# Kernel tuning notes

Measured on AMD Instinct MI355X. Metric: run time of the kernel, lower is better.

The kernel has to match this reference:

```python
import jax, jax.numpy as jnp
import numpy as np

QLEN, MLEN, D, H = 1024, 1024, 1024, 16
DH = D // H
KLEN = QLEN + MLEN
SCALE = 1.0 / np.sqrt(DH).astype(np.float32)
W_STD = 0.02


def setup_inputs() -> dict:
    key = jax.random.key(0)
    ks = jax.random.split(key, 14)
    inputs = jax.random.normal(ks[0], (QLEN, 1, D), jnp.float32)
    r = jax.random.normal(ks[1], (KLEN, D), jnp.float32)
    u = jax.random.normal(ks[2], (H, DH), jnp.float32) * W_STD
    v = jax.random.normal(ks[3], (H, DH), jnp.float32) * W_STD
    mem = jax.random.normal(ks[4], (MLEN, 1, D), jnp.float32)
    # causal mask over concatenated [mem, inputs] keys: True = masked
    attn_mask = jnp.triu(jnp.ones((QLEN, KLEN), bool), k=MLEN + 1)
    W_qkv = jax.random.normal(ks[5], (3 * D, D), jnp.float32) * W_STD
    W_r = jax.random.normal(ks[6], (D, D), jnp.float32) * W_STD
    W_o = jax.random.normal(ks[7], (D, D), jnp.float32) * W_STD
    W_ih = jax.random.normal(ks[8], (3 * D, D), jnp.float32) * W_STD
    W_hh = jax.random.normal(ks[9], (3 * D, D), jnp.float32) * W_STD
    b_ih = jnp.zeros((3 * D,), jnp.float32)
    b_hh = jnp.zeros((3 * D,), jnp.float32)
    h0 = jnp.zeros((1, 1, D), jnp.float32)  # GRU hidden, forces batch=1
    return {"inputs": inputs, "r": r, "u": u, "v": v, "attn_mask": attn_mask,
            "mem": mem, "W_qkv": W_qkv, "W_r": W_r, "W_o": W_o,
            "W_ih": W_ih, "W_hh": W_hh, "b_ih": b_ih, "b_hh": b_hh, "h0": h0}


def _rel_shift(x):
    # Transformer-XL relative shift; x: [qlen, klen, b, n]
    q, k, b, n = x.shape
    zp = jnp.zeros((q, 1, b, n), x.dtype)
    xp = jnp.concatenate([zp, x], axis=1)          # [q, k+1, b, n]
    xp = xp.reshape(k + 1, q, b, n)[1:]            # drop first row
    return xp.reshape(q, k, b, n)


def reference(inputs, r, u, v, attn_mask, mem, W_qkv, W_r, W_o,
              W_ih, W_hh, b_ih, b_hh, h0):
    qlen, b, d = inputs.shape
    cat = jnp.concatenate([mem, inputs], axis=0)        # [klen, b, d]
    klen = cat.shape[0]
    w_heads = cat @ W_qkv.T                             # [klen, b, 3d]
    q_h, k_h, v_h = jnp.split(w_heads, 3, axis=-1)
    q_h = q_h[-qlen:].reshape(qlen, b, H, DH)
    k_h = k_h.reshape(klen, b, H, DH)
    v_h = v_h.reshape(klen, b, H, DH)
    r_k = (r @ W_r.T).reshape(klen, H, DH)              # relative key heads

    AC = jnp.einsum('ibnd,jbnd->ijbn', q_h + u, k_h)    # content score
    BD = _rel_shift(jnp.einsum('ibnd,jnd->ijbn', q_h + v, r_k))  # position score
    score = (AC + BD) * SCALE                           # [q, k, b, n]
    score = jnp.where(attn_mask[:, :, None, None], jnp.float32(-1e30), score)
    probs = jax.nn.softmax(score, axis=1)

    attn_vec = jnp.einsum('ijbn,jbnd->ibnd', probs, v_h).reshape(qlen, b, d)
    y = attn_vec @ W_o.T                                # [q, b, d]

    # 1-layer GRU over time (PyTorch gate order r, z, n)
    x_proj = y @ W_ih.T + b_ih                          # [q, b, 3d]

    def step(h, xt):
        gh = h @ W_hh.T + b_hh
        xr, xz, xn = jnp.split(xt, 3, axis=-1)
        hr, hz, hn = jnp.split(gh, 3, axis=-1)
        rg = jax.nn.sigmoid(xr + hr)
        zg = jax.nn.sigmoid(xz + hz)
        ng = jnp.tanh(xn + rg * hn)
        h_new = (1.0 - zg) * ng + zg * h
        return h_new, h_new

    _, ys = jax.lax.scan(step, h0[0], x_proj)           # h0[0]: [b, d]
    return ys, probs
```

## Files before the change

kernel.cpp:

```cpp
#include <hip/hip_runtime.h>
#include <hip/hip_bf16.h>
#include <math.h>

#define QL   1024
#define ML   1024
#define KL   2048
#define DM   1024
#define NH   16
#define DH   64
#define SCL  0.125f
#define GRU_BLOCKS 128
#define GRU_ELPB   8

typedef __attribute__((ext_vector_type(8))) short bfrag;
typedef __attribute__((ext_vector_type(4))) float facc;

static __device__ __forceinline__ float dot4(const float4& a, const float4& b) {
    return a.x*b.x + a.y*b.y + a.z*b.z + a.w*b.w;
}

static __device__ __forceinline__ unsigned bf16_rne(float x) {
    unsigned u = __float_as_uint(x);
    return (u + 0x7FFF + ((u >> 16) & 1)) >> 16;
}
static __device__ __forceinline__ void bfsplit(float a, short& h, short& l) {
    unsigned uh = bf16_rne(a);
    h = (short)uh;
    float ah = __uint_as_float(uh << 16);
    l = (short)bf16_rne(a - ah);
}

static __device__ __forceinline__ void gemm_body(
    const float* __restrict__ A, const float* __restrict__ A2, int asplit,
    const float* __restrict__ B, const float* __restrict__ bias,
    float* __restrict__ C, int N, int K, int bx, int by)
{
    __shared__ short Ah[128*40], Al[128*40], Bh[128*40], Bl[128*40];
    const int tid = threadIdx.x;
    const int wv = tid >> 6, ln = tid & 63;
    const int wr = wv >> 1, wc = wv & 1;
    const int lm = ln & 15, lk = ln >> 4;
    facc acc[4][4] = {};

    const int srow = tid >> 1;
    const int scol = (tid & 1) << 4;
    const int arow = by*128 + srow;
    const float* Ap = ((A2 && arow >= asplit)
                        ? A2 + (size_t)(arow - asplit)*K
                        : A  + (size_t)arow*K) + scol;
    const float* Bp = B + (size_t)(bx*128 + srow)*K + scol;

    float4 ar[4], br[4];
    #pragma unroll
    for (int c = 0; c < 4; c++) {
        ar[c] = *(const float4*)(Ap + c*4);
        br[c] = *(const float4*)(Bp + c*4);
    }

    for (int k0 = 0; k0 < K; k0 += 32) {
        bfrag a_h0, a_h1, a_l0, a_l1, b_h0, b_h1, b_l0, b_l1;
        #pragma unroll
        for (int c = 0; c < 4; c++) {
            const float av[4] = {ar[c].x, ar[c].y, ar[c].z, ar[c].w};
            const float bv[4] = {br[c].x, br[c].y, br[c].z, br[c].w};
            #pragma unroll
            for (int q = 0; q < 4; q++) {
                const int e = c*4 + q;
                short h, l;
                bfsplit(av[q], h, l);
                if (e < 8) { a_h0[e] = h; a_l0[e] = l; }
                else       { a_h1[e-8] = h; a_l1[e-8] = l; }
                bfsplit(bv[q], h, l);
                if (e < 8) { b_h0[e] = h; b_l0[e] = l; }
                else       { b_h1[e-8] = h; b_l1[e-8] = l; }
            }
        }
        __syncthreads();
        *(bfrag*)&Ah[srow*40 + scol    ] = a_h0;
        *(bfrag*)&Ah[srow*40 + scol + 8] = a_h1;
        *(bfrag*)&Al[srow*40 + scol    ] = a_l0;
        *(bfrag*)&Al[srow*40 + scol + 8] = a_l1;
        *(bfrag*)&Bh[srow*40 + scol    ] = b_h0;
        *(bfrag*)&Bh[srow*40 + scol + 8] = b_h1;
        *(bfrag*)&Bl[srow*40 + scol    ] = b_l0;
        *(bfrag*)&Bl[srow*40 + scol + 8] = b_l1;
        __syncthreads();
        if (k0 + 32 < K) {
            #pragma unroll
            for (int c = 0; c < 4; c++) {
                ar[c] = *(const float4*)(Ap + k0 + 32 + c*4);
                br[c] = *(const float4*)(Bp + k0 + 32 + c*4);
            }
        }
        bfrag fah[4], fal[4], fbh[4], fbl[4];
        #pragma unroll
        for (int i = 0; i < 4; i++) {
            const int rA = wr*64 + i*16 + lm;
            fah[i] = *(const bfrag*)&Ah[rA*40 + lk*8];
            fal[i] = *(const bfrag*)&Al[rA*40 + lk*8];
            const int rB = wc*64 + i*16 + lm;
            fbh[i] = *(const bfrag*)&Bh[rB*40 + lk*8];
            fbl[i] = *(const bfrag*)&Bl[rB*40 + lk*8];
        }
        #pragma unroll
        for (int i = 0; i < 4; i++)
            #pragma unroll
            for (int j = 0; j < 4; j++) {
                acc[i][j] = __builtin_amdgcn_mfma_f32_16x16x32_bf16(fah[i], fbh[j], acc[i][j], 0, 0, 0);
                acc[i][j] = __builtin_amdgcn_mfma_f32_16x16x32_bf16(fah[i], fbl[j], acc[i][j], 0, 0, 0);
                acc[i][j] = __builtin_amdgcn_mfma_f32_16x16x32_bf16(fal[i], fbh[j], acc[i][j], 0, 0, 0);
            }
    }

    const int m0 = by*128 + wr*64 + lk*4;
    const int n0 = bx*128 + wc*64 + lm;
    #pragma unroll
    for (int j = 0; j < 4; j++) {
        const float bj = bias ? bias[n0 + j*16] : 0.f;
        #pragma unroll
        for (int i = 0; i < 4; i++)
            #pragma unroll
            for (int r = 0; r < 4; r++)
                C[(size_t)(m0 + i*16 + r)*N + n0 + j*16] = acc[i][j][r] + bj;
    }
}

__global__ __launch_bounds__(256) void gemm_nt_mfma(
    const float* __restrict__ A, const float* __restrict__ B,
    const float* __restrict__ bias, float* __restrict__ C,
    int N, int K)
{
    gemm_body(A, nullptr, 1<<30, B, bias, C, N, K, blockIdx.x, blockIdx.y);
}

__global__ __launch_bounds__(256) void gemm_fused_qkv_rk(
    const float* __restrict__ mem, const float* __restrict__ inputs,
    const float* __restrict__ Wqkv, float* __restrict__ wheads,
    const float* __restrict__ r_in, const float* __restrict__ Wr,
    float* __restrict__ rk)
{
    int blk = blockIdx.x;
    if (blk < 384) {
        const int bx = blk % 24, by = blk / 24;
        if (by < 8 && bx < 8) return;
        gemm_body(mem, inputs, 8*128, Wqkv, nullptr, wheads, 3072, DM, bx, by);
    } else {
        blk -= 384;
        const int bx = blk % 8, by = blk / 8;
        gemm_body(r_in, nullptr, 1<<30, Wr, nullptr, rk, 1024, DM, bx, by);
    }
}

__global__ __launch_bounds__(256) void wd_kernel(
    const float* __restrict__ rk, const float* __restrict__ u_,
    const float* __restrict__ v_, float* __restrict__ wd)
{
    int idx = blockIdx.x*256 + threadIdx.x;
    if (idx >= NH*KL) return;
    int n = idx >> 11, jr = idx & (KL-1);
    const float* rp = rk + (size_t)jr*DM + n*DH;
    const float* up = u_ + n*DH;
    const float* vp = v_ + n*DH;
    float s = 0.f;
    #pragma unroll
    for (int d4 = 0; d4 < 16; d4++) {
        float4 r4 = *(const float4*)(rp + d4*4);
        float4 uu = *(const float4*)(up + d4*4);
        float4 vv = *(const float4*)(vp + d4*4);
        s += (vv.x-uu.x)*r4.x + (vv.y-uu.y)*r4.y + (vv.z-uu.z)*r4.z + (vv.w-uu.w)*r4.w;
    }
    wd[idx] = s;
}

__global__ __launch_bounds__(256) void score_kernel(
    const float* __restrict__ wh, const float* __restrict__ rk,
    const float* __restrict__ u_, const float* __restrict__ wd,
    float* __restrict__ sc)
{
    const int jt = blockIdx.x, it = blockIdx.y, n = blockIdx.z;
    const int i0 = it*64, j0 = jt*64;
    if (j0 > i0 + 1087) return;
    __shared__ float squ[64*64];
    __shared__ float sk [64*64];
    __shared__ float sr [128*64];
    __shared__ float swd[128];
    const int tid = threadIdx.x;
    #pragma unroll
    for (int rr = 0; rr < 4; rr++) {
        int p = tid + 256*rr;
        int row = p >> 4, c4 = p & 15;
        int phys = (c4 ^ ((row >> 2) & 15)) << 2;
        float4 q4 = *(const float4*)&wh[(size_t)(ML + i0 + row)*3072 + n*DH + (c4<<2)];
        float4 u4 = *(const float4*)&u_[n*DH + (c4<<2)];
        float4 t4; t4.x=q4.x+u4.x; t4.y=q4.y+u4.y; t4.z=q4.z+u4.z; t4.w=q4.w+u4.w;
        *(float4*)&squ[row*64 + phys] = t4;
        float4 k4 = *(const float4*)&wh[(size_t)(j0 + row)*3072 + DM + n*DH + (c4<<2)];
        *(float4*)&sk[row*64 + phys] = k4;
    }
    const int jr0 = j0 - i0 + 960;
    #pragma unroll
    for (int rr = 0; rr < 8; rr++) {
        int p = tid + 256*rr;
        int row = p >> 4, c4 = p & 15;
        int phys = (c4 ^ ((row >> 2) & 15)) << 2;
        int jr = jr0 + row;
        float4 r4;
        if (jr >= 0 && jr < KL) r4 = *(const float4*)&rk[(size_t)jr*DM + n*DH + (c4<<2)];
        else { r4.x = r4.y = r4.z = r4.w = 0.f; }
        *(float4*)&sr[row*64 + phys] = r4;
    }
    if (tid < 128) {
        int jr = jr0 + tid;
        swd[tid] = (jr >= 0 && jr < KL) ? wd[n*KL + jr] : 0.f;
    }
    __syncthreads();

    const int tj2 = tid & 15, ti2 = tid >> 4;
    const int rbase = tj2*4 - ti2*4 + 60;
    float acc[4][4] = {};
    #pragma unroll
    for (int dc = 0; dc < 16; dc++) {
        float4 qa[4], kb[4], rv[7];
        #pragma unroll
        for (int a = 0; a < 4; a++) {
            int row = ti2*4 + a;
            qa[a] = *(const float4*)&squ[row*64 + ((dc ^ ((row>>2)&15)) << 2)];
        }
        #pragma unroll
        for (int b_ = 0; b_ < 4; b_++) {
            int row = tj2*4 + b_;
            kb[b_] = *(const float4*)&sk[row*64 + ((dc ^ ((row>>2)&15)) << 2)];
        }
        #pragma unroll
        for (int o = 0; o < 7; o++) {
            int row = rbase + o;
            rv[o] = *(const float4*)&sr[row*64 + ((dc ^ ((row>>2)&15)) << 2)];
        }
        #pragma unroll
        for (int a = 0; a < 4; a++)
            #pragma unroll
            for (int b_ = 0; b_ < 4; b_++)
                acc[a][b_] += dot4(qa[a], kb[b_]) + dot4(qa[a], rv[3 + b_ - a]);
    }
    #pragma unroll
    for (int a = 0; a < 4; a++) {
        int i = i0 + ti2*4 + a;
        float4 o;
        o.x = (acc[a][0] + swd[rbase + 3 + 0 - a]) * SCL;
        o.y = (acc[a][1] + swd[rbase + 3 + 1 - a]) * SCL;
        o.z = (acc[a][2] + swd[rbase + 3 + 2 - a]) * SCL;
        o.w = (acc[a][3] + swd[rbase + 3 + 3 - a]) * SCL;
        *(float4*)&sc[((size_t)i*NH + n)*KL + j0 + (tj2<<2)] = o;
    }
}

__global__ __launch_bounds__(512) void softmaxT_kernel(float* __restrict__ sc)
{
    const int i = blockIdx.x;
    const int tid = threadIdx.x;
    __shared__ float ld[16*2052];
    __shared__ float sinv[16];
    float* slab = sc + (size_t)i*KL*NH;
    #pragma unroll
    for (int rr = 0; rr < 16; rr++) {
        int p = tid + 512*rr;
        int nn = p >> 9, j = (p & 511) << 2;
        float4 f = *(const float4*)(slab + ((size_t)nn << 11) + j);
        *(float4*)&ld[nn*2052 + j] = f;
    }
    __syncthreads();
    const int g = tid >> 5, tl = tid & 31;
    const int jmax = i + ML;
    float m = -3.4e38f;
    for (int k = 0; k < 64; k++) {
        int j = tl + (k << 5);
        if (j <= jmax) m = fmaxf(m, ld[g*2052 + j]);
    }
    #pragma unroll
    for (int off = 1; off <= 16; off <<= 1) m = fmaxf(m, __shfl_xor(m, off, 64));
    float ssum = 0.f;
    for (int k = 0; k < 64; k++) {
        int j = tl + (k << 5);
        float e = 0.f;
        if (j <= jmax) { e = __expf(ld[g*2052 + j] - m); ssum += e; }
        ld[g*2052 + j] = e;
    }
    #pragma unroll
    for (int off = 1; off <= 16; off <<= 1) ssum += __shfl_xor(ssum, off, 64);
    if (tl == 0) sinv[g] = 1.f / ssum;
    __syncthreads();
    #pragma unroll
    for (int rr = 0; rr < 16; rr++) {
        int p = tid + 512*rr;
        int j = p >> 2, n0 = (p & 3) << 2;
        float4 o;
        o.x = ld[(n0+0)*2052 + j] * sinv[n0+0];
        o.y = ld[(n0+1)*2052 + j] * sinv[n0+1];
        o.z = ld[(n0+2)*2052 + j] * sinv[n0+2];
        o.w = ld[(n0+3)*2052 + j] * sinv[n0+3];
        *(float4*)(slab + (size_t)p*4) = o;
    }
}

__global__ __launch_bounds__(512) void pv_kernel(
    const float* __restrict__ sc, const float* __restrict__ wh,
    float* __restrict__ attn)
{
    const int it = blockIdx.x >> 1, dh = blockIdx.x & 1;
    const int i0 = it*8;
    const int tid = threadIdx.x;
    __shared__ float Ps[8*16*20];
    __shared__ float Vs[16][512];
    const int col = dh*512 + tid;
    const int nn = col >> 6;
    float acc[8] = {};
    const int jlast = i0 + 7 + ML;
    const int nch = (jlast + 16) >> 4;
    for (int ch = 0; ch < nch; ch++) {
        const int j0 = ch << 4;
        __syncthreads();
        {
            int ii = tid >> 6, rem = tid & 63, jj = rem >> 2, n0 = (rem & 3) << 2;
            float4 f = *(const float4*)(sc + ((size_t)(i0+ii)*KL + j0 + jj)*NH + n0);
            Ps[(ii*16 + n0+0)*20 + jj] = f.x;
            Ps[(ii*16 + n0+1)*20 + jj] = f.y;
            Ps[(ii*16 + n0+2)*20 + jj] = f.z;
            Ps[(ii*16 + n0+3)*20 + jj] = f.w;
        }
        #pragma unroll
        for (int rr = 0; rr < 4; rr++) {
            int p = tid + 512*rr;
            int row = p >> 7, c4 = (p & 127) << 2;
            float4 f = *(const float4*)&wh[(size_t)(j0+row)*3072 + 2048 + dh*512 + c4];
            *(float4*)&Vs[row][c4] = f;
        }
        __syncthreads();
        #pragma unroll
        for (int jq = 0; jq < 4; jq++) {
            float4 pv[8];
            #pragma unroll
            for (int ii = 0; ii < 8; ii++)
                pv[ii] = *(const float4*)&Ps[(ii*16 + nn)*20 + jq*4];
            #pragma unroll
            for (int jj = 0; jj < 4; jj++) {
                float vv = Vs[jq*4 + jj][tid];
                #pragma unroll
                for (int ii = 0; ii < 8; ii++)
                    acc[ii] += ((const float*)&pv[ii])[jj] * vv;
            }
        }
    }
    #pragma unroll
    for (int ii = 0; ii < 8; ii++)
        attn[(size_t)(i0+ii)*DM + col] = acc[ii];
}

__global__ __launch_bounds__(512) void gru_persistent(
    const float* __restrict__ xp,
    const float* __restrict__ Whh,
    const float* __restrict__ bhh,
    const float* __restrict__ h0,
    float* __restrict__ ys,
    unsigned long long* __restrict__ hpack)
{
    __shared__ float wlds[3][GRU_ELPB][DM];
    __shared__ float hlds[DM];
    const int b = blockIdx.x;
    const int tid = threadIdx.x;
    const int w = tid >> 6, l = tid & 63;
    const int dg = b*GRU_ELPB + w;

    #pragma unroll
    for (int k = 0; k < 12; k++) {
        int idx = tid + 512*k;
        int g   = idx >> 11;
        int rem = idx & 2047;
        int e   = rem >> 8;
        int c   = rem & 255;
        float4 f = *(const float4*)&Whh[(size_t)(g*DM + b*GRU_ELPB + e)*DM + (c<<2)];
        *(float4*)&wlds[g][e][c<<2] = f;
    }
    float bh0=0.f, bh1=0.f, bh2=0.f, hreg=0.f;
    if (l == 0) {
        bh0 = bhh[dg]; bh1 = bhh[dg + DM]; bh2 = bhh[dg + 2*DM];
        hreg = h0[dg];
    }

    bool bail = false;
    for (int t = 0; t < QL; t++) {
        float xr=0.f, xz=0.f, xn=0.f;
        if (l == 0) {
            const float* xrow = xp + (size_t)t*3072 + dg;
            xr = xrow[0]; xz = xrow[DM]; xn = xrow[2*DM];
        }
        if (t == 0) {
            hlds[tid]       = h0[tid];
            hlds[tid + 512] = h0[tid + 512];
        } else if (!bail) {
            const unsigned long long* hp = hpack + ((size_t)(t & 1) << 10);
            unsigned long long v0 = 0, v1 = 0;
            bool d0 = false, d1 = false;
            int guard = 0;
            for (;;) {
                if (!d0) { v0 = __hip_atomic_load(&hp[tid],       __ATOMIC_RELAXED, __HIP_MEMORY_SCOPE_AGENT);
                           d0 = (unsigned)(v0 >> 32) >= (unsigned)t; }
                if (!d1) { v1 = __hip_atomic_load(&hp[tid + 512], __ATOMIC_RELAXED, __HIP_MEMORY_SCOPE_AGENT);
                           d1 = (unsigned)(v1 >> 32) >= (unsigned)t; }
                if (d0 && d1) break;
                if (++guard > (1<<18)) { bail = true; break; }
            }
            hlds[tid]       = __uint_as_float((unsigned)v0);
            hlds[tid + 512] = __uint_as_float((unsigned)v1);
        }
        __syncthreads();

        float s0=0.f, s1=0.f, s2=0.f;
        #pragma unroll
        for (int c = 0; c < 4; c++) {
            const int base = c*256 + l*4;
            float4 h4 = *(const float4*)&hlds[base];
            float4 w0 = *(const float4*)&wlds[0][w][base];
            float4 w1 = *(const float4*)&wlds[1][w][base];
            float4 w2 = *(const float4*)&wlds[2][w][base];
            s0 += dot4(w0, h4);
            s1 += dot4(w1, h4);
            s2 += dot4(w2, h4);
        }
        #pragma unroll
        for (int off = 32; off >= 1; off >>= 1) {
            s0 += __shfl_xor(s0, off, 64);
            s1 += __shfl_xor(s1, off, 64);
            s2 += __shfl_xor(s2, off, 64);
        }
        if (l == 0) {
            const float hr = s0 + bh0;
            const float hz = s1 + bh1;
            const float hn = s2 + bh2;
            const float rg = 1.f/(1.f + __expf(-(xr + hr)));
            const float zg = 1.f/(1.f + __expf(-(xz + hz)));
            const float e2 = __expf(2.f*(xn + rg*hn));
            const float ng = (e2 - 1.f) / (e2 + 1.f);
            const float hnew = (1.f - zg)*ng + zg*hreg;
            hreg = hnew;
            unsigned long long pk = (unsigned long long)__float_as_uint(hnew)
                                  | ((unsigned long long)(unsigned)(t+1) << 32);
            __hip_atomic_store(&hpack[(((size_t)(t+1) & 1) << 10) + dg], pk,
                               __ATOMIC_RELAXED, __HIP_MEMORY_SCOPE_AGENT);
            ys[(size_t)t*DM + dg] = hnew;
        }
    }
}

extern "C" void kernel_launch(void* const* d_in, const int* in_sizes, int n_in,
                              void* d_out, int out_size, void* d_ws, size_t ws_size,
                              hipStream_t stream) {
    const float* inputs = (const float*)d_in[0];
    const float* r_in   = (const float*)d_in[1];
    const float* u_in   = (const float*)d_in[2];
    const float* v_in   = (const float*)d_in[3];
    const float* mem    = (const float*)d_in[5];
    const float* Wqkv   = (const float*)d_in[6];
    const float* Wr     = (const float*)d_in[7];
    const float* Wo     = (const float*)d_in[8];
    const float* Wih    = (const float*)d_in[9];
    const float* Whh    = (const float*)d_in[10];
    const float* b_ih   = (const float*)d_in[11];
    const float* b_hh   = (const float*)d_in[12];
    const float* h0     = (const float*)d_in[13];

    float* out = (float*)d_out;
    float* ys  = out;
    float* sc  = out + (size_t)QL*DM;

    float* ws      = (float*)d_ws;
    float* cat     = ws;
    float* wheads  = cat    + (size_t)KL*DM;
    float* rk      = wheads + (size_t)KL*3072;
    float* wd      = rk     + (size_t)KL*DM;
    float* attn    = wd     + (size_t)NH*KL;
    float* ybuf    = attn   + (size_t)QL*DM;
    float* xproj   = ybuf   + (size_t)QL*DM;
    unsigned long long* hpack = (unsigned long long*)(xproj + (size_t)QL*3072);

    hipMemsetAsync(hpack, 0, 2*DM*sizeof(unsigned long long), stream);

    gemm_fused_qkv_rk<<<512, 256, 0, stream>>>(mem, inputs, Wqkv, wheads, r_in, Wr, rk);
    wd_kernel<<<128, 256, 0, stream>>>(rk, u_in, v_in, wd);
    score_kernel<<<dim3(32,16,16), 256, 0, stream>>>(wheads, rk, u_in, wd, sc);
    softmaxT_kernel<<<QL, 512, 0, stream>>>(sc);
    pv_kernel<<<256, 512, 0, stream>>>(sc, wheads, attn);
    gemm_nt_mfma<<<dim3(8,8), 256, 0, stream>>>(attn, Wo, nullptr, ybuf, DM, DM);
    gemm_nt_mfma<<<dim3(24,8), 256, 0, stream>>>(ybuf, Wih, b_ih, xproj, 3072, DM);
    gru_persistent<<<GRU_BLOCKS, 512, 0, stream>>>(xproj, Whh, b_hh, h0, ys, hpack);
}
```

Measured before the change: 2.813 ms.

## Fuse input-projection GEMM into persistent GRU kernel with per-row-block readiness flags

The x_proj GEMM moves into the same launch as the persistent GRU kernel: 192 extra blocks compute 128-row tiles of x_proj and bump a per-row-block counter, and the GRU blocks spin on the counter before consuming each 128-step chunk. This overlaps the GEMM with the start of the sequential recurrence and removes one kernel launch. GEMM blocks run 512 threads where only 256 do the work, so the rest idle through matching barriers. Correctness depends on the GRU blocks and GEMM blocks being co-resident, and the spin has a guard that bails out on timeout.

```diff
diff --git a/kernel.cpp b/kernel.cpp
--- a/kernel.cpp
+++ b/kernel.cpp
@@ -355,18 +355,39 @@
         attn[(size_t)(i0+ii)*DM + col] = acc[ii];
 }
 
-__global__ __launch_bounds__(512) void gru_persistent(
-    const float* __restrict__ xp,
+__global__ __launch_bounds__(512) void gru_xproj_fused(
+    const float* __restrict__ ybuf,
+    const float* __restrict__ Wih,
+    const float* __restrict__ bih,
+    float* __restrict__ xproj,
     const float* __restrict__ Whh,
     const float* __restrict__ bhh,
     const float* __restrict__ h0,
     float* __restrict__ ys,
-    unsigned long long* __restrict__ hpack)
-{
+    unsigned long long* __restrict__ hpack,
+    unsigned* __restrict__ xdone)
+{
+    const int blk = blockIdx.x;
+    const int tid = threadIdx.x;
+
+    if (blk >= GRU_BLOCKS) {
+        const int gblk = blk - GRU_BLOCKS;
+        const int bx = gblk % 24, by = gblk / 24;
+        if (tid < 256) {
+            gemm_body(ybuf, nullptr, 1<<30, Wih, bih, xproj, 3072, DM, bx, by);
+        } else {
+            for (int k0 = 0; k0 < DM; k0 += 32) { __syncthreads(); __syncthreads(); }
+        }
+        __syncthreads();
+        if (tid == 0)
+            __hip_atomic_fetch_add(&xdone[by], 1u, __ATOMIC_RELEASE,
+                                   __HIP_MEMORY_SCOPE_AGENT);
+        return;
+    }
+
     __shared__ float wlds[3][GRU_ELPB][DM];
     __shared__ float hlds[DM];
-    const int b = blockIdx.x;
-    const int tid = threadIdx.x;
+    const int b = blk;
     const int w = tid >> 6, l = tid & 63;
     const int dg = b*GRU_ELPB + w;
 
@@ -387,10 +408,23 @@
     }
 
     bool bail = false;
+    int ready_by = -1;
     for (int t = 0; t < QL; t++) {
+        const int need = t >> 7;
+        if (need > ready_by) {
+            if (l == 0) {
+                int guard = 0;
+                while (__hip_atomic_load(&xdone[need], __ATOMIC_RELAXED,
+                                         __HIP_MEMORY_SCOPE_AGENT) < 24u) {
+                    if (++guard > (1<<18)) break;
+                }
+                __builtin_amdgcn_fence(__ATOMIC_ACQUIRE, "agent");
+            }
+            ready_by = need;
+        }
         float xr=0.f, xz=0.f, xn=0.f;
         if (l == 0) {
-            const float* xrow = xp + (size_t)t*3072 + dg;
+            const float* xrow = xproj + (size_t)t*3072 + dg;
             xr = xrow[0]; xz = xrow[DM]; xn = xrow[2*DM];
         }
         if (t == 0) {
@@ -481,8 +515,9 @@
     float* ybuf    = attn   + (size_t)QL*DM;
     float* xproj   = ybuf   + (size_t)QL*DM;
     unsigned long long* hpack = (unsigned long long*)(xproj + (size_t)QL*3072);
-
-    hipMemsetAsync(hpack, 0, 2*DM*sizeof(unsigned long long), stream);
+    unsigned* xdone = (unsigned*)(hpack + 2*DM);
+
+    hipMemsetAsync(hpack, 0, 2*DM*sizeof(unsigned long long) + 8*sizeof(unsigned), stream);
 
     gemm_fused_qkv_rk<<<512, 256, 0, stream>>>(mem, inputs, Wqkv, wheads, r_in, Wr, rk);
     wd_kernel<<<128, 256, 0, stream>>>(rk, u_in, v_in, wd);
@@ -490,6 +525,6 @@
     softmaxT_kernel<<<QL, 512, 0, stream>>>(sc);
     pv_kernel<<<256, 512, 0, stream>>>(sc, wheads, attn);
     gemm_nt_mfma<<<dim3(8,8), 256, 0, stream>>>(attn, Wo, nullptr, ybuf, DM, DM);
-    gemm_nt_mfma<<<dim3(24,8), 256, 0, stream>>>(ybuf, Wih, b_ih, xproj, 3072, DM);
-    gru_persistent<<<GRU_BLOCKS, 512, 0, stream>>>(xproj, Whh, b_hh, h0, ys, hpack);
-}
+    gru_xproj_fused<<<GRU_BLOCKS + 192, 512, 0, stream>>>(
+        ybuf, Wih, b_ih, xproj, Whh, b_hh, h0, ys, hpack, xdone);
+}
```

Result: no change. 2.859 ms (+1.6%).
